# Kernel tuning notes

Measured on AMD Instinct MI355X. Metric: run time of the kernel, lower is better.

Reference implementation:

```python
import jax, jax.numpy as jnp
import numpy as np

TEMP = 0.07
BASE_TEMP = 0.07
EPS = 1e-8


def setup_inputs() -> dict:
    key = jax.random.key(0)
    features = jax.random.normal(key, (4096, 2, 128), dtype=jnp.float32)
    return {"features": features}


def reference(features):
    B, V, D = features.shape  # bsz, n_views, dim
    # torch.cat(torch.unbind(features, dim=1), dim=0): view-major ordering
    cf = jnp.swapaxes(features, 0, 1).reshape(V * B, D)  # [N, D], N = V*B
    # cosine similarity = normalize rows then GEMM (same math as broadcasted CosineSimilarity)
    n = cf / jnp.maximum(jnp.linalg.norm(cf, axis=-1, keepdims=True), EPS)
    logits = jnp.matmul(n, n.T) / TEMP  # [N, N]
    N = V * B
    logits_mask = 1.0 - jnp.eye(N, dtype=logits.dtype)  # zero out self-contrast
    # SimCLR mask: eye(B) tiled over (anchor_count, contrast_count), minus diagonal
    pos_mask = jnp.tile(jnp.eye(B, dtype=logits.dtype), (V, V)) * logits_mask
    exp_logits = jnp.exp(logits) * logits_mask
    log_prob = logits - jnp.log(exp_logits.sum(axis=1, keepdims=True))
    mean_log_prob_pos = (pos_mask * log_prob).sum(axis=1) / pos_mask.sum(axis=1)
    loss = -(TEMP / BASE_TEMP) * mean_log_prob_pos
    return loss.reshape(V, B).mean()
```

## Files before the change

kernel.cpp:

```cpp
#include <hip/hip_runtime.h>
#include <hip/hip_bf16.h>
#include <math.h>


constexpr int   Bsz   = 4096;
constexpr int   Nrows = 8192;
constexpr int   Dd    = 128;
constexpr float TEMPf = 0.07f;
constexpr float EPSN  = 1e-8f;
constexpr float SCALE = 1.4426950408889634f / 0.07f;
constexpr float LN2   = 0.6931471805599453f;

constexpr int CHUNKS     = 32;
constexpr int CHUNK_COLS = Nrows / CHUNKS;
constexpr int TILES      = CHUNK_COLS / 32;
constexpr int ROWS_BLK   = 256;
constexpr int NPAIRS     = CHUNKS * (CHUNKS + 1) / 2;
constexpr int YG         = Nrows / ROWS_BLK;
constexpr int PREPBLKS   = Bsz / 4;

typedef __attribute__((ext_vector_type(8)))  short bf16x8;
typedef __attribute__((ext_vector_type(16))) float floatx16;


constexpr size_t OFF_PART = 0x200000;
constexpr size_t OFF_SPOS = 0x300000;

__global__ void prep_k(const float* __restrict__ f,
                       char* __restrict__ nF,
                       float* __restrict__ sposPart,
                       float* __restrict__ out) {
    __shared__ float sred[4];
    int tid  = threadIdx.x;
    int wid  = tid >> 6;
    int lane = tid & 63;
    int b    = blockIdx.x * 4 + wid;
    if (blockIdx.x == 0 && tid == 0) out[0] = 0.f;

    const float* s0 = f + (size_t)(b * 2) * Dd;
    float2 x = *(const float2*)(s0 + lane * 2);
    float2 y = *(const float2*)(s0 + Dd + lane * 2);
    float ss0 = x.x * x.x + x.y * x.y;
    float ss1 = y.x * y.x + y.y * y.y;
    float dt  = x.x * y.x + x.y * y.y;
    #pragma unroll
    for (int off = 32; off; off >>= 1) {
        ss0 += __shfl_xor(ss0, off);
        ss1 += __shfl_xor(ss1, off);
        dt  += __shfl_xor(dt,  off);
    }
    float inv0 = 1.0f / fmaxf(sqrtf(ss0), EPSN);
    float inv1 = 1.0f / fmaxf(sqrtf(ss1), EPSN);

    size_t poff = (size_t)(lane >> 3) * 1024 + ((lane >> 2) & 1) * 512
                + (lane & 3) * 4;

    __hip_bfloat162 h;
    h.x = __float2bfloat16(x.x * inv0);
    h.y = __float2bfloat16(x.y * inv0);
    *(__hip_bfloat162*)(nF + (size_t)(b >> 5) * 8192 + (b & 31) * 16 + poff) = h;
    int r1 = Bsz + b;
    h.x = __float2bfloat16(y.x * inv1);
    h.y = __float2bfloat16(y.y * inv1);
    *(__hip_bfloat162*)(nF + (size_t)(r1 >> 5) * 8192 + (r1 & 31) * 16 + poff) = h;

    if (lane == 0) sred[wid] = dt * inv0 * inv1 / TEMPf;
    __syncthreads();
    if (tid == 0) sposPart[blockIdx.x] = sred[0] + sred[1] + sred[2] + sred[3];
}

__device__ __forceinline__ void load_tile(bf16x8* dst, const char* gB, int t,
                                          int lane) {
    #pragma unroll
    for (int kc = 0; kc < 8; kc++)
        dst[kc] = *(const bf16x8*)(gB + (size_t)t * 8192 + kc * 1024 + lane * 16);
}

__global__ __launch_bounds__(256, 2)
void main_k(const char* __restrict__ nF, float* __restrict__ partial) {
    __shared__ float colred[4][256];
    __shared__ float rred[256];
    const int tid  = threadIdx.x;
    const int wid  = tid >> 6;
    const int lane = tid & 63;
    const int lo   = lane & 31;
    const int hi   = lane >> 5;

    int p = blockIdx.x, ci = 0;
    while (p >= CHUNKS - ci) { p -= CHUNKS - ci; ci++; }
    const int cj = ci + p;

    const int rbase = ci * ROWS_BLK + wid * 64;
    const int cbase = cj * ROWS_BLK;
    const char* gB  = nF + (size_t)(cj * 8) * 8192;

    bf16x8 afrag[2][8];
    #pragma unroll
    for (int s = 0; s < 2; s++) {
        const char* ag = nF + (size_t)((rbase + s * 32) >> 5) * 8192 + lane * 16;
        #pragma unroll
        for (int kc = 0; kc < 8; kc++)
            afrag[s][kc] = *(const bf16x8*)(ag + kc * 1024);
    }

    float rs[2][16];
    #pragma unroll
    for (int s = 0; s < 2; s++)
        #pragma unroll
        for (int r = 0; r < 16; r++) rs[s][r] = 0.f;

    auto compute = [&](const bf16x8 (&bf)[8], int t) {
        floatx16 acc0 = {}, acc1 = {};
        #pragma unroll
        for (int kc = 0; kc < 8; kc++) {
            acc0 = __builtin_amdgcn_mfma_f32_32x32x16_bf16(afrag[0][kc], bf[kc], acc0, 0, 0, 0);
            acc1 = __builtin_amdgcn_mfma_f32_32x32x16_bf16(afrag[1][kc], bf[kc], acc1, 0, 0, 0);
        }
        const int cb32 = cbase + t * 32;
        float cs = 0.f;
        #pragma unroll
        for (int s = 0; s < 2; s++) {
            const floatx16& acc = s ? acc1 : acc0;
            if (cb32 == rbase + s * 32) {
                #pragma unroll
                for (int r = 0; r < 16; r++) {
                    float e = __builtin_amdgcn_exp2f(acc[r] * SCALE);
                    if (lo == ((r & 3) + 8 * (r >> 2) + 4 * hi)) e = 0.f;
                    cs += e; rs[s][r] += e;
                }
            } else {
                #pragma unroll
                for (int r = 0; r < 16; r++) {
                    float e = __builtin_amdgcn_exp2f(acc[r] * SCALE);
                    cs += e; rs[s][r] += e;
                }
            }
        }
        cs += __shfl_xor(cs, 32);
        if (hi == 0) colred[wid][t * 32 + lo] = cs;
    };

    bf16x8 bA[8], bB[8];
    load_tile(bA, gB, 0, lane);
    #pragma unroll 1
    for (int t = 0; t < TILES; t += 2) {
        load_tile(bB, gB, t + 1, lane);
        compute(bA, t);
        if (t + 2 < TILES) load_tile(bA, gB, t + 2, lane);
        compute(bB, t + 1);
    }

    if (ci != cj) {
        #pragma unroll
        for (int s = 0; s < 2; s++) {
            #pragma unroll
            for (int r = 0; r < 16; r++) {
                float v = rs[s][r];
                v += __shfl_xor(v, 1);
                v += __shfl_xor(v, 2);
                v += __shfl_xor(v, 4);
                v += __shfl_xor(v, 8);
                v += __shfl_xor(v, 16);
                if (lo == r)
                    rred[wid * 64 + s * 32 + ((r & 3) + 8 * (r >> 2) + 4 * hi)] = v;
            }
        }
    }

    __syncthreads();
    float v = colred[0][tid] + colred[1][tid] + colred[2][tid] + colred[3][tid];
    partial[(size_t)ci * Nrows + cbase + tid] = v;
    if (ci != cj)
        partial[(size_t)cj * Nrows + ci * ROWS_BLK + tid] = rred[tid];
}

__global__ __launch_bounds__(256)
void final_k(const float* __restrict__ partial, const float* __restrict__ sposPart,
             float* __restrict__ out) {
    __shared__ float red[4];
    int tid = threadIdx.x;
    int r = blockIdx.x * 256 + tid;
    float se = 0.f;
    #pragma unroll
    for (int p = 0; p < YG; p++) se += partial[(size_t)p * Nrows + r];
    float acc = __builtin_amdgcn_logf(se) * LN2;
    if (tid < 32) acc -= 2.f * sposPart[blockIdx.x * 32 + tid];
    #pragma unroll
    for (int off = 32; off; off >>= 1) acc += __shfl_xor(acc, off);
    if ((tid & 63) == 0) red[tid >> 6] = acc;
    __syncthreads();
    if (tid == 0)
        atomicAdd(out, (red[0] + red[1] + red[2] + red[3]) / (float)Nrows);
}

extern "C" void kernel_launch(void* const* d_in, const int* in_sizes, int n_in,
                              void* d_out, int out_size, void* d_ws, size_t ws_size,
                              hipStream_t stream) {
    const float* f = (const float*)d_in[0];
    char* ws = (char*)d_ws;
    char* nF        = ws;
    float* partial  = (float*)(ws + OFF_PART);
    float* sposPart = (float*)(ws + OFF_SPOS);

    prep_k<<<PREPBLKS, 256, 0, stream>>>(f, nF, sposPart, (float*)d_out);
    main_k<<<NPAIRS, 256, 0, stream>>>(nF, partial);
    final_k<<<Nrows / 256, 256, 0, stream>>>(partial, sposPart, (float*)d_out);
}
```

Measured before the change: 87.05 us.

## Stage B tiles through LDS with async global_load_lds double buffering

Replaces the per-wave register loading of B tiles, where every wave loaded the full tile, with a cooperative async global-to-LDS copy. Each wave loads a quarter of the tile into a double-buffered shared buffer, and all waves read fragments from LDS. This cuts redundant global/L2 traffic and register pressure, so launch bounds are raised to target three blocks per CU. In exchange it adds a __syncthreads per tile and LDS read latency. It also relies on the single barrier being enough to order the async LDS writes before they are consumed.

```diff
diff --git a/kernel.cpp b/kernel.cpp
--- a/kernel.cpp
+++ b/kernel.cpp
@@ -25,6 +25,12 @@
 
 constexpr size_t OFF_PART = 0x200000;
 constexpr size_t OFF_SPOS = 0x300000;
+
+__device__ __forceinline__ void gld_lds16(const void* g, void* l) {
+    __builtin_amdgcn_global_load_lds(
+        (const __attribute__((address_space(1))) void*)g,
+        (__attribute__((address_space(3))) void*)l, 16, 0, 0);
+}
 
 __global__ void prep_k(const float* __restrict__ f,
                        char* __restrict__ nF,
@@ -69,15 +75,9 @@
     if (tid == 0) sposPart[blockIdx.x] = sred[0] + sred[1] + sred[2] + sred[3];
 }
 
-__device__ __forceinline__ void load_tile(bf16x8* dst, const char* gB, int t,
-                                          int lane) {
-    #pragma unroll
-    for (int kc = 0; kc < 8; kc++)
-        dst[kc] = *(const bf16x8*)(gB + (size_t)t * 8192 + kc * 1024 + lane * 16);
-}
-
-__global__ __launch_bounds__(256, 2)
+__global__ __launch_bounds__(256, 3)
 void main_k(const char* __restrict__ nF, float* __restrict__ partial) {
+    __shared__ char  bufs[2][8192];
     __shared__ float colred[4][256];
     __shared__ float rred[256];
     const int tid  = threadIdx.x;
@@ -92,7 +92,7 @@
 
     const int rbase = ci * ROWS_BLK + wid * 64;
     const int cbase = cj * ROWS_BLK;
-    const char* gB  = nF + (size_t)(cj * 8) * 8192;
+    const int cg0   = cj * 8;
 
     bf16x8 afrag[2][8];
     #pragma unroll
@@ -109,13 +109,33 @@
         #pragma unroll
         for (int r = 0; r < 16; r++) rs[s][r] = 0.f;
 
-    auto compute = [&](const bf16x8 (&bf)[8], int t) {
+    {
+        const char* g0 = nF + (size_t)cg0 * 8192;
+        int kc = wid * 2;
+        gld_lds16(g0 + kc * 1024 + lane * 16,       &bufs[0][kc * 1024]);
+        gld_lds16(g0 + (kc + 1) * 1024 + lane * 16, &bufs[0][(kc + 1) * 1024]);
+    }
+
+    #pragma unroll 1
+    for (int t = 0; t < TILES; t++) {
+        __syncthreads();
+        if (t + 1 < TILES) {
+            const char* gn = nF + (size_t)(cg0 + t + 1) * 8192;
+            char* dst = bufs[(t + 1) & 1];
+            int kc = wid * 2;
+            gld_lds16(gn + kc * 1024 + lane * 16,       dst + kc * 1024);
+            gld_lds16(gn + (kc + 1) * 1024 + lane * 16, dst + (kc + 1) * 1024);
+        }
+
+        const char* buf = bufs[t & 1];
         floatx16 acc0 = {}, acc1 = {};
         #pragma unroll
         for (int kc = 0; kc < 8; kc++) {
-            acc0 = __builtin_amdgcn_mfma_f32_32x32x16_bf16(afrag[0][kc], bf[kc], acc0, 0, 0, 0);
-            acc1 = __builtin_amdgcn_mfma_f32_32x32x16_bf16(afrag[1][kc], bf[kc], acc1, 0, 0, 0);
-        }
+            bf16x8 bf = *(const bf16x8*)&buf[kc * 1024 + lane * 16];
+            acc0 = __builtin_amdgcn_mfma_f32_32x32x16_bf16(afrag[0][kc], bf, acc0, 0, 0, 0);
+            acc1 = __builtin_amdgcn_mfma_f32_32x32x16_bf16(afrag[1][kc], bf, acc1, 0, 0, 0);
+        }
+
         const int cb32 = cbase + t * 32;
         float cs = 0.f;
         #pragma unroll
@@ -138,16 +158,6 @@
         }
         cs += __shfl_xor(cs, 32);
         if (hi == 0) colred[wid][t * 32 + lo] = cs;
-    };
-
-    bf16x8 bA[8], bB[8];
-    load_tile(bA, gB, 0, lane);
-    #pragma unroll 1
-    for (int t = 0; t < TILES; t += 2) {
-        load_tile(bB, gB, t + 1, lane);
-        compute(bA, t);
-        if (t + 2 < TILES) load_tile(bA, gB, t + 2, lane);
-        compute(bB, t + 1);
     }
 
     if (ci != cj) {
```

Result: faster. 81.15 us (-6.8%).
